# Kernel optimization log

Measured on AMD Instinct MI355X. Metric: run time of the kernel, lower is better.

## Reference

```python
import jax, jax.numpy as jnp
import numpy as np

N_NODES = 100000
N_EDGES = 800000
IN_DIM = 128
NUM_HEADS = 8
HEAD_DIM = 16  # out_dim // num_heads = 128 // 8


def setup_inputs() -> dict:
    key = jax.random.key(0)
    ks = jax.random.split(key, 10)
    scale = 1.0 / np.sqrt(IN_DIM)
    return {
        "x": jax.random.normal(ks[0], (N_NODES, IN_DIM), dtype=jnp.float32),
        "edge_index": jax.random.randint(ks[1], (2, N_EDGES), 0, N_NODES, dtype=jnp.int64),
        "virt_h": jax.random.normal(ks[2], (1, IN_DIM), dtype=jnp.float32),
        "virt_edge_index": jax.random.randint(ks[3], (2, 1), 0, 1, dtype=jnp.int64),
        "Wq": jax.random.normal(ks[4], (IN_DIM, NUM_HEADS * HEAD_DIM), dtype=jnp.float32) * scale,
        "bq": jnp.zeros((NUM_HEADS * HEAD_DIM,), dtype=jnp.float32),
        "Wk": jax.random.normal(ks[5], (IN_DIM, NUM_HEADS * HEAD_DIM), dtype=jnp.float32) * scale,
        "bk": jnp.zeros((NUM_HEADS * HEAD_DIM,), dtype=jnp.float32),
        "Wv": jax.random.normal(ks[6], (IN_DIM, NUM_HEADS * HEAD_DIM), dtype=jnp.float32) * scale,
        "bv": jnp.zeros((NUM_HEADS * HEAD_DIM,), dtype=jnp.float32),
    }


def reference(x, edge_index, virt_h, virt_edge_index, Wq, bq, Wk, bk, Wv, bv):
    # use_virt_nodes=False: virt_h / virt_edge_index are unused dummies.
    n = x.shape[0]
    H, D = NUM_HEADS, HEAD_DIM
    Q = (x @ Wq + bq).reshape(n, H, D)
    K = (x @ Wk + bk).reshape(n, H, D)
    V = (x @ Wv + bv).reshape(n, H, D)

    src = edge_index[0]
    dst = edge_index[1]

    # edge-wise gather QK dot -> clamp -> exp; score: [E, H, 1]
    dot = jnp.sum(K[src] * Q[dst], axis=-1, keepdims=True) / np.sqrt(D).astype(np.float32)
    score = jnp.exp(jnp.clip(dot, -5.0, 5.0))

    msg = V[src] * score  # [E, H, D]
    wV = jax.ops.segment_sum(msg, dst, num_segments=n)     # [N, H, D]
    Z = jax.ops.segment_sum(score, dst, num_segments=n)    # [N, H, 1]

    h_out = (wV / (Z + 1e-6)).reshape(n, H * D)
    return h_out
```

## Files before the change

### kernel.cpp

```cpp
#include <hip/hip_runtime.h>

#define IN_DIM   128
#define NH       8
#define HD       16
#define OUTD     128
#define QKVD     384

typedef unsigned short ushort_t;
typedef unsigned int   uint_t;
typedef __bf16 bf16x8 __attribute__((ext_vector_type(8)));
typedef float  f32x4  __attribute__((ext_vector_type(4)));
typedef unsigned short us4 __attribute__((ext_vector_type(4)));

__device__ __forceinline__ float bf2f(ushort_t u) {
    return __uint_as_float(((uint_t)u) << 16);
}
__device__ __forceinline__ ushort_t f2bf(float f) {
    uint_t u = __float_as_uint(f);
    u += 0x7FFFu + ((u >> 16) & 1u);
    return (ushort_t)(u >> 16);
}

__global__ __launch_bounds__(256) void prep_w(
    const float* __restrict__ Wq, const float* __restrict__ Wk,
    const float* __restrict__ Wv, ushort_t* __restrict__ Wt,
    int* __restrict__ P, unsigned long long* __restrict__ desc, int N)
{
    __shared__ float ld[32][33];
    int mat  = blockIdx.x >> 4;
    int tile = blockIdx.x & 15;
    int k0 = (tile >> 2) * 32, c0 = (tile & 3) * 32;
    const float* W = (mat == 0) ? Wq : (mat == 1) ? Wk : Wv;
    int t = threadIdx.x;
    {
        int k = t >> 3, c4 = (t & 7) * 4;
        float4 f = *(const float4*)&W[(size_t)(k0 + k) * 128 + c0 + c4];
        ld[k][c4 + 0] = f.x; ld[k][c4 + 1] = f.y;
        ld[k][c4 + 2] = f.z; ld[k][c4 + 3] = f.w;
    }
    __syncthreads();
    {
        int c = t >> 3, kg = (t & 7) * 4;
        union { ushort_t h[4]; uint2 u; } o;
        o.h[0] = f2bf(ld[kg + 0][c]); o.h[1] = f2bf(ld[kg + 1][c]);
        o.h[2] = f2bf(ld[kg + 2][c]); o.h[3] = f2bf(ld[kg + 3][c]);
        *(uint2*)&Wt[((size_t)(mat * 128 + c0 + c)) * 128 + k0 + kg] = o.u;
    }
    int t0 = blockIdx.x * 256 + threadIdx.x;
    for (int i = t0; i < N; i += 48 * 256) P[i] = 0;
    if (t0 < 128) desc[t0] = 0ULL;
}

__global__ __launch_bounds__(384, 3) void gemm_rank(
    const float* __restrict__ x, const ushort_t* __restrict__ Wt,
    const float* __restrict__ bq, const float* __restrict__ bk,
    const float* __restrict__ bv,
    const int* __restrict__ ei, int* __restrict__ P,
    ushort_t* __restrict__ rank,
    ushort_t* __restrict__ qkv,
    int N, int E, int ntiles)
{
    {
        int gtid   = (int)blockIdx.x * 384 + threadIdx.x;
        int stride = (int)gridDim.x * 384;
        for (int e = gtid; e < E; e += stride) {
            int d = ei[E + e];
            int old = atomicAdd(&P[d], 1);
            rank[e] = (ushort_t)old;
        }
    }

    __shared__ ushort_t sh[8320];

    const int tid  = threadIdx.x;
    const int w    = tid >> 6;
    const int quad = (tid >> 4) & 3;
    const int l15  = tid & 15;
    const int colg = w << 6;

    bf16x8 bfr[4][4];
#pragma unroll
    for (int kt = 0; kt < 4; kt++)
#pragma unroll
        for (int cs = 0; cs < 4; cs++) {
            int col = colg + cs * 16 + l15;
            bfr[kt][cs] = *(const bf16x8*)&Wt[(size_t)col * 128 + kt * 32 + quad * 8];
        }

    const int mat = w >> 1;
    const float* Bp = (mat == 0) ? bq : (mat == 1) ? bk : bv;
    float bias[4];
#pragma unroll
    for (int cs = 0; cs < 4; cs++)
        bias[cs] = Bp[((w & 1) << 6) + cs * 16 + l15];

    for (int tile = blockIdx.x; tile < ntiles; tile += gridDim.x) {
        const int row0 = tile * 64;
        __syncthreads();

        for (int ch = tid; ch < 1024; ch += 384) {
            int row = ch >> 4;
            int kc  = ch & 15;
            int grow = row0 + row; if (grow > N - 1) grow = N - 1;
            const float* xp = x + (size_t)grow * IN_DIM + kc * 8;
            float4 f0 = *(const float4*)xp;
            float4 f1 = *(const float4*)(xp + 4);
            union { ushort_t h[8]; uint4 u; } tt;
            tt.h[0] = f2bf(f0.x); tt.h[1] = f2bf(f0.y);
            tt.h[2] = f2bf(f0.z); tt.h[3] = f2bf(f0.w);
            tt.h[4] = f2bf(f1.x); tt.h[5] = f2bf(f1.y);
            tt.h[6] = f2bf(f1.z); tt.h[7] = f2bf(f1.w);
            *(uint4*)&sh[(kc * 65 + row) * 8] = tt.u;
        }
        __syncthreads();

        f32x4 acc[4][4];
#pragma unroll
        for (int r = 0; r < 4; r++)
#pragma unroll
            for (int cs = 0; cs < 4; cs++) acc[r][cs] = (f32x4){0.f, 0.f, 0.f, 0.f};

#pragma unroll
        for (int kt = 0; kt < 4; kt++) {
            int kc = kt * 4 + quad;
            bf16x8 af[4];
#pragma unroll
            for (int r = 0; r < 4; r++)
                af[r] = *(const bf16x8*)&sh[(kc * 65 + r * 16 + l15) * 8];
#pragma unroll
            for (int r = 0; r < 4; r++)
#pragma unroll
                for (int cs = 0; cs < 4; cs++)
                    acc[r][cs] = __builtin_amdgcn_mfma_f32_16x16x32_bf16(
                        af[r], bfr[kt][cs], acc[r][cs], 0, 0, 0);
        }

#define EPS 392
#pragma unroll
        for (int qq = 0; qq < 4; qq++) {
            __syncthreads();
            int lrow = quad << 2;
#pragma unroll
            for (int cs = 0; cs < 4; cs++) {
                int col = (w << 6) + cs * 16 + l15;
#pragma unroll
                for (int reg = 0; reg < 4; reg++)
                    sh[(lrow + reg) * EPS + col] = f2bf(acc[qq][cs][reg] + bias[cs]);
            }
            __syncthreads();
#pragma unroll
            for (int i = 0; i < 2; i++) {
                int c = tid + i * 384;
                int row = c / 48;
                int col = (c % 48) * 8;
                int grow = row0 + qq * 16 + row;
                if (grow < N) {
                    uint4 val = *(const uint4*)&sh[row * EPS + col];
                    *(uint4*)&qkv[(size_t)grow * QKVD + col] = val;
                }
            }
        }
#undef EPS
    }
}

__global__ __launch_bounds__(1024) void scan_onepass(
    int* __restrict__ P, unsigned long long* __restrict__ desc, int N)
{
    __shared__ int sdata[1024];
    __shared__ int s_prefix;
    int b = blockIdx.x;
    int i = b * 1024 + threadIdx.x;
    int v = (i < N) ? P[i] : 0;
    sdata[threadIdx.x] = v;
    __syncthreads();
    for (int off = 1; off < 1024; off <<= 1) {
        int t = (threadIdx.x >= off) ? sdata[threadIdx.x - off] : 0;
        __syncthreads();
        sdata[threadIdx.x] += t;
        __syncthreads();
    }
    int incl  = sdata[threadIdx.x];
    int total = sdata[1023];

    if (threadIdx.x == 0) {
        unsigned long long st1 = ((unsigned long long)((b == 0) ? 2 : 1) << 32)
                                 | (uint_t)total;
        __hip_atomic_store(&desc[b], st1, __ATOMIC_RELEASE, __HIP_MEMORY_SCOPE_AGENT);
        int prefix = 0;
        if (b > 0) {
            int bb = b - 1;
            for (;;) {
                unsigned long long d = __hip_atomic_load(
                    &desc[bb], __ATOMIC_ACQUIRE, __HIP_MEMORY_SCOPE_AGENT);
                uint_t st = (uint_t)(d >> 32);
                if (st == 0) continue;
                prefix += (int)(uint_t)(d & 0xFFFFFFFFu);
                if (st == 2) break;
                bb--;
            }
            __hip_atomic_store(&desc[b],
                ((unsigned long long)2 << 32) | (uint_t)(prefix + total),
                __ATOMIC_RELEASE, __HIP_MEMORY_SCOPE_AGENT);
        }
        s_prefix = prefix;
    }
    __syncthreads();
    if (i < N) P[i] = s_prefix + incl - v;
}

__global__ __launch_bounds__(256) void scatter(
    const int* __restrict__ ei, const int* __restrict__ P,
    const ushort_t* __restrict__ rank,
    int* __restrict__ sorted_src, int E)
{
    int e0 = (blockIdx.x * 256 + threadIdx.x) * 4;
    if (e0 + 4 <= E) {
        int4 s4 = *(const int4*)&ei[e0];
        int4 d4 = *(const int4*)&ei[E + e0];
        us4  r4 = *(const us4*)&rank[e0];
        sorted_src[P[d4.x] + (int)r4[0]] = s4.x;
        sorted_src[P[d4.y] + (int)r4[1]] = s4.y;
        sorted_src[P[d4.z] + (int)r4[2]] = s4.z;
        sorted_src[P[d4.w] + (int)r4[3]] = s4.w;
    } else {
        for (int e = e0; e < E; e++) {
            int pos = P[ei[E + e]] + (int)rank[e];
            sorted_src[pos] = ei[e];
        }
    }
}

__global__ __launch_bounds__(256) void segment_attn(
    const ushort_t* __restrict__ qkv,
    const int* __restrict__ P, const int* __restrict__ sorted_src,
    float* __restrict__ out, int N, int E)
{
    int n = (blockIdx.x * 256 + threadIdx.x) >> 4;
    int g = threadIdx.x & 15;
    if (n >= N) return;
    int start = P[n];
    int end   = (n + 1 < N) ? P[n + 1] : E;
    int deg   = end - start;

    const uint_t* qrow = (const uint_t*)(qkv + (size_t)n * QKVD);
    uint4 qu = *(const uint4*)(qrow + g * 4);
    float q0 = bf2f((ushort_t)(qu.x & 0xFFFF)), q1 = bf2f((ushort_t)(qu.x >> 16));
    float q2 = bf2f((ushort_t)(qu.y & 0xFFFF)), q3 = bf2f((ushort_t)(qu.y >> 16));
    float q4 = bf2f((ushort_t)(qu.z & 0xFFFF)), q5 = bf2f((ushort_t)(qu.z >> 16));
    float q6 = bf2f((ushort_t)(qu.w & 0xFFFF)), q7 = bf2f((ushort_t)(qu.w >> 16));

    float a0 = 0.f, a1 = 0.f, a2 = 0.f, a3 = 0.f;
    float a4 = 0.f, a5 = 0.f, a6 = 0.f, a7 = 0.f, z = 0.f;

    int myidx = (g < deg) ? sorted_src[start + g] : 0;
    int wbase = (threadIdx.x & 63) & 48;

#define PROC(ku, vu)                                                       \
    {                                                                      \
        float p = bf2f((ushort_t)((ku).x & 0xFFFF)) * q0                   \
                + bf2f((ushort_t)((ku).x >> 16))    * q1                   \
                + bf2f((ushort_t)((ku).y & 0xFFFF)) * q2                   \
                + bf2f((ushort_t)((ku).y >> 16))    * q3                   \
                + bf2f((ushort_t)((ku).z & 0xFFFF)) * q4                   \
                + bf2f((ushort_t)((ku).z >> 16))    * q5                   \
                + bf2f((ushort_t)((ku).w & 0xFFFF)) * q6                   \
                + bf2f((ushort_t)((ku).w >> 16))    * q7;                  \
        p += __shfl_xor(p, 1);                                             \
        p = fminf(fmaxf(p * 0.25f, -5.f), 5.f);                            \
        float s = __expf(p);                                               \
        a0 += bf2f((ushort_t)((vu).x & 0xFFFF)) * s;                       \
        a1 += bf2f((ushort_t)((vu).x >> 16))    * s;                       \
        a2 += bf2f((ushort_t)((vu).y & 0xFFFF)) * s;                       \
        a3 += bf2f((ushort_t)((vu).y >> 16))    * s;                       \
        a4 += bf2f((ushort_t)((vu).z & 0xFFFF)) * s;                       \
        a5 += bf2f((ushort_t)((vu).z >> 16))    * s;                       \
        a6 += bf2f((ushort_t)((vu).w & 0xFFFF)) * s;                       \
        a7 += bf2f((ushort_t)((vu).w >> 16))    * s;                       \
        z += s;                                                            \
    }

    int cnt = (deg < 16) ? deg : 16;
    int t = 0;
    for (; t + 2 <= cnt; t += 2) {
        int s0 = __shfl(myidx, wbase + t);
        int s1 = __shfl(myidx, wbase + t + 1);
        const uint_t* kv0 = (const uint_t*)(qkv + (size_t)s0 * QKVD + 128);
        const uint_t* kv1 = (const uint_t*)(qkv + (size_t)s1 * QKVD + 128);
        uint4 ku0 = *(const uint4*)(kv0 + g * 4);
        uint4 ku1 = *(const uint4*)(kv1 + g * 4);
        uint4 vu0 = *(const uint4*)(kv0 + 64 + g * 4);
        uint4 vu1 = *(const uint4*)(kv1 + 64 + g * 4);
        PROC(ku0, vu0); PROC(ku1, vu1);
    }
    if (t < cnt) {
        int s0 = __shfl(myidx, wbase + t);
        const uint_t* kv0 = (const uint_t*)(qkv + (size_t)s0 * QKVD + 128);
        uint4 ku0 = *(const uint4*)(kv0 + g * 4);
        uint4 vu0 = *(const uint4*)(kv0 + 64 + g * 4);
        PROC(ku0, vu0);
    }
    for (int j = start + 16; j < end; j++) {
        int s0 = sorted_src[j];
        const uint_t* kv0 = (const uint_t*)(qkv + (size_t)s0 * QKVD + 128);
        uint4 ku0 = *(const uint4*)(kv0 + g * 4);
        uint4 vu0 = *(const uint4*)(kv0 + 64 + g * 4);
        PROC(ku0, vu0);
    }
#undef PROC

    float inv = 1.f / (z + 1e-6f);
    float4 o0 = {a0 * inv, a1 * inv, a2 * inv, a3 * inv};
    float4 o1 = {a4 * inv, a5 * inv, a6 * inv, a7 * inv};
    float* ob = out + (size_t)n * OUTD + g * 8;
    *(float4*)ob = o0;
    *(float4*)(ob + 4) = o1;
}

extern "C" void kernel_launch(void* const* d_in, const int* in_sizes, int n_in,
                              void* d_out, int out_size, void* d_ws, size_t ws_size,
                              hipStream_t stream) {
    const float* x  = (const float*)d_in[0];
    const int*   ei = (const int*)d_in[1];
    const float* Wq = (const float*)d_in[4];
    const float* bq = (const float*)d_in[5];
    const float* Wk = (const float*)d_in[6];
    const float* bk = (const float*)d_in[7];
    const float* Wv = (const float*)d_in[8];
    const float* bv = (const float*)d_in[9];
    float* out = (float*)d_out;

    const int N = in_sizes[0] / IN_DIM;
    const int E = in_sizes[1] / 2;

    char* wsb = (char*)d_ws;
    ushort_t* qkv = (ushort_t*)wsb;
    ushort_t* Wt  = qkv + (size_t)N * QKVD;
    int* P = (int*)(Wt + 384 * 128);
    unsigned long long* desc = (unsigned long long*)((char*)P + (size_t)N * 4);
    int* sorted = (int*)((char*)desc + 1024);
    ushort_t* rank = (ushort_t*)(sorted + E);

    const int ntiles = (N + 63) / 64;
    const int NB     = (N + 1023) / 1024;

    prep_w<<<48, 256, 0, stream>>>(Wq, Wk, Wv, Wt, P, desc, N);
    gemm_rank<<<512, 384, 0, stream>>>(
        x, Wt, bq, bk, bv, ei, P, rank, qkv, N, E, ntiles);
    scan_onepass<<<NB, 1024, 0, stream>>>(P, desc, N);
    scatter<<<(E / 4 + 255) / 256, 256, 0, stream>>>(ei, P, rank, sorted, E);
    segment_attn<<<((size_t)N * 16 + 255) / 256, 256, 0, stream>>>(
        qkv, P, sorted, out, N, E);
}
```

Before: 284.5 us.

## Replace global-atomic counting sort with two-level bucketed sort by destination

Edge sorting by destination no longer uses per-edge global atomics plus rank arrays. It now runs a block-local histogram over 128-node buckets, a scan over the bucket-by-block table, a bucketing pass with LDS atomics that packs src and the low dst bits, and a per-bucket fine sort that writes the CSR offsets and the sorted sources. This aims to cut contended global atomics and random global scatter. In exchange it adds kernels, separates the GEMM from the edge counting so the two no longer overlap, and needs an extra bucket buffer. The packed format also assumes source indices fit in 20 bits.

```diff
diff --git a/kernel.cpp b/kernel.cpp
--- a/kernel.cpp
+++ b/kernel.cpp
@@ -5,12 +5,12 @@
 #define HD       16
 #define OUTD     128
 #define QKVD     384
+#define SH       7
 
 typedef unsigned short ushort_t;
 typedef unsigned int   uint_t;
 typedef __bf16 bf16x8 __attribute__((ext_vector_type(8)));
 typedef float  f32x4  __attribute__((ext_vector_type(4)));
-typedef unsigned short us4 __attribute__((ext_vector_type(4)));
 
 __device__ __forceinline__ float bf2f(ushort_t u) {
     return __uint_as_float(((uint_t)u) << 16);
@@ -24,7 +24,7 @@
 __global__ __launch_bounds__(256) void prep_w(
     const float* __restrict__ Wq, const float* __restrict__ Wk,
     const float* __restrict__ Wv, ushort_t* __restrict__ Wt,
-    int* __restrict__ P, unsigned long long* __restrict__ desc, int N)
+    unsigned long long* __restrict__ desc)
 {
     __shared__ float ld[32][33];
     int mat  = blockIdx.x >> 4;
@@ -47,121 +47,23 @@
         *(uint2*)&Wt[((size_t)(mat * 128 + c0 + c)) * 128 + k0 + kg] = o.u;
     }
     int t0 = blockIdx.x * 256 + threadIdx.x;
-    for (int i = t0; i < N; i += 48 * 256) P[i] = 0;
     if (t0 < 128) desc[t0] = 0ULL;
 }
 
-__global__ __launch_bounds__(384, 3) void gemm_rank(
-    const float* __restrict__ x, const ushort_t* __restrict__ Wt,
-    const float* __restrict__ bq, const float* __restrict__ bk,
-    const float* __restrict__ bv,
-    const int* __restrict__ ei, int* __restrict__ P,
-    ushort_t* __restrict__ rank,
-    ushort_t* __restrict__ qkv,
-    int N, int E, int ntiles)
-{
-    {
-        int gtid   = (int)blockIdx.x * 384 + threadIdx.x;
-        int stride = (int)gridDim.x * 384;
-        for (int e = gtid; e < E; e += stride) {
-            int d = ei[E + e];
-            int old = atomicAdd(&P[d], 1);
-            rank[e] = (ushort_t)old;
-        }
-    }
-
-    __shared__ ushort_t sh[8320];
-
-    const int tid  = threadIdx.x;
-    const int w    = tid >> 6;
-    const int quad = (tid >> 4) & 3;
-    const int l15  = tid & 15;
-    const int colg = w << 6;
-
-    bf16x8 bfr[4][4];
-#pragma unroll
-    for (int kt = 0; kt < 4; kt++)
-#pragma unroll
-        for (int cs = 0; cs < 4; cs++) {
-            int col = colg + cs * 16 + l15;
-            bfr[kt][cs] = *(const bf16x8*)&Wt[(size_t)col * 128 + kt * 32 + quad * 8];
-        }
-
-    const int mat = w >> 1;
-    const float* Bp = (mat == 0) ? bq : (mat == 1) ? bk : bv;
-    float bias[4];
-#pragma unroll
-    for (int cs = 0; cs < 4; cs++)
-        bias[cs] = Bp[((w & 1) << 6) + cs * 16 + l15];
-
-    for (int tile = blockIdx.x; tile < ntiles; tile += gridDim.x) {
-        const int row0 = tile * 64;
-        __syncthreads();
-
-        for (int ch = tid; ch < 1024; ch += 384) {
-            int row = ch >> 4;
-            int kc  = ch & 15;
-            int grow = row0 + row; if (grow > N - 1) grow = N - 1;
-            const float* xp = x + (size_t)grow * IN_DIM + kc * 8;
-            float4 f0 = *(const float4*)xp;
-            float4 f1 = *(const float4*)(xp + 4);
-            union { ushort_t h[8]; uint4 u; } tt;
-            tt.h[0] = f2bf(f0.x); tt.h[1] = f2bf(f0.y);
-            tt.h[2] = f2bf(f0.z); tt.h[3] = f2bf(f0.w);
-            tt.h[4] = f2bf(f1.x); tt.h[5] = f2bf(f1.y);
-            tt.h[6] = f2bf(f1.z); tt.h[7] = f2bf(f1.w);
-            *(uint4*)&sh[(kc * 65 + row) * 8] = tt.u;
-        }
-        __syncthreads();
-
-        f32x4 acc[4][4];
-#pragma unroll
-        for (int r = 0; r < 4; r++)
-#pragma unroll
-            for (int cs = 0; cs < 4; cs++) acc[r][cs] = (f32x4){0.f, 0.f, 0.f, 0.f};
-
-#pragma unroll
-        for (int kt = 0; kt < 4; kt++) {
-            int kc = kt * 4 + quad;
-            bf16x8 af[4];
-#pragma unroll
-            for (int r = 0; r < 4; r++)
-                af[r] = *(const bf16x8*)&sh[(kc * 65 + r * 16 + l15) * 8];
-#pragma unroll
-            for (int r = 0; r < 4; r++)
-#pragma unroll
-                for (int cs = 0; cs < 4; cs++)
-                    acc[r][cs] = __builtin_amdgcn_mfma_f32_16x16x32_bf16(
-                        af[r], bfr[kt][cs], acc[r][cs], 0, 0, 0);
-        }
-
-#define EPS 392
-#pragma unroll
-        for (int qq = 0; qq < 4; qq++) {
-            __syncthreads();
-            int lrow = quad << 2;
-#pragma unroll
-            for (int cs = 0; cs < 4; cs++) {
-                int col = (w << 6) + cs * 16 + l15;
-#pragma unroll
-                for (int reg = 0; reg < 4; reg++)
-                    sh[(lrow + reg) * EPS + col] = f2bf(acc[qq][cs][reg] + bias[cs]);
-            }
-            __syncthreads();
-#pragma unroll
-            for (int i = 0; i < 2; i++) {
-                int c = tid + i * 384;
-                int row = c / 48;
-                int col = (c % 48) * 8;
-                int grow = row0 + qq * 16 + row;
-                if (grow < N) {
-                    uint4 val = *(const uint4*)&sh[row * EPS + col];
-                    *(uint4*)&qkv[(size_t)grow * QKVD + col] = val;
-                }
-            }
-        }
-#undef EPS
-    }
+__global__ __launch_bounds__(256) void ehist(
+    const int* __restrict__ ei, int* __restrict__ Hf, int E, int NBC)
+{
+    __shared__ int lh[1024];
+    for (int i = threadIdx.x; i < 1024; i += 256) lh[i] = 0;
+    __syncthreads();
+    int CH = (E + 127) >> 7;
+    int e0 = blockIdx.x * CH;
+    int e1 = min(E, e0 + CH);
+    for (int e = e0 + threadIdx.x; e < e1; e += 256)
+        atomicAdd(&lh[ei[E + e] >> SH], 1);
+    __syncthreads();
+    for (int b = threadIdx.x; b < NBC; b += 256)
+        Hf[b * 128 + blockIdx.x] = lh[b];
 }
 
 __global__ __launch_bounds__(1024) void scan_onepass(
@@ -209,25 +111,161 @@
     if (i < N) P[i] = s_prefix + incl - v;
 }
 
-__global__ __launch_bounds__(256) void scatter(
-    const int* __restrict__ ei, const int* __restrict__ P,
-    const ushort_t* __restrict__ rank,
-    int* __restrict__ sorted_src, int E)
-{
-    int e0 = (blockIdx.x * 256 + threadIdx.x) * 4;
-    if (e0 + 4 <= E) {
-        int4 s4 = *(const int4*)&ei[e0];
-        int4 d4 = *(const int4*)&ei[E + e0];
-        us4  r4 = *(const us4*)&rank[e0];
-        sorted_src[P[d4.x] + (int)r4[0]] = s4.x;
-        sorted_src[P[d4.y] + (int)r4[1]] = s4.y;
-        sorted_src[P[d4.z] + (int)r4[2]] = s4.z;
-        sorted_src[P[d4.w] + (int)r4[3]] = s4.w;
-    } else {
-        for (int e = e0; e < E; e++) {
-            int pos = P[ei[E + e]] + (int)rank[e];
-            sorted_src[pos] = ei[e];
-        }
+__global__ __launch_bounds__(256) void ebucket(
+    const int* __restrict__ ei, const int* __restrict__ S,
+    uint_t* __restrict__ bkt, int E, int NBC)
+{
+    __shared__ int lb[1024];
+    for (int b = threadIdx.x; b < NBC; b += 256)
+        lb[b] = S[b * 128 + blockIdx.x];
+    __syncthreads();
+    int CH = (E + 127) >> 7;
+    int e0 = blockIdx.x * CH;
+    int e1 = min(E, e0 + CH);
+    for (int e = e0 + threadIdx.x; e < e1; e += 256) {
+        int d   = ei[E + e];
+        int src = ei[e];
+        int pos = atomicAdd(&lb[d >> SH], 1);
+        bkt[pos] = (uint_t)src | ((uint_t)(d & 127) << 20);
+    }
+}
+
+__global__ __launch_bounds__(256) void efine(
+    const uint_t* __restrict__ bkt, const int* __restrict__ S,
+    int* __restrict__ P, int* __restrict__ sorted_src,
+    int E, int N, int NBC)
+{
+    __shared__ int cnt[128];
+    __shared__ int scn[128];
+    int b    = blockIdx.x;
+    int base = S[b * 128];
+    int end  = (b + 1 < NBC) ? S[(b + 1) * 128] : E;
+    int m    = end - base;
+    if (threadIdx.x < 128) cnt[threadIdx.x] = 0;
+    __syncthreads();
+    for (int i = threadIdx.x; i < m; i += 256)
+        atomicAdd(&cnt[bkt[base + i] >> 20], 1);
+    __syncthreads();
+    if (threadIdx.x < 128) scn[threadIdx.x] = cnt[threadIdx.x];
+    __syncthreads();
+    for (int off = 1; off < 128; off <<= 1) {
+        int v = (threadIdx.x >= off && threadIdx.x < 128) ? scn[threadIdx.x - off] : 0;
+        __syncthreads();
+        if (threadIdx.x < 128) scn[threadIdx.x] += v;
+        __syncthreads();
+    }
+    if (threadIdx.x < 128) {
+        int excl = scn[threadIdx.x] - cnt[threadIdx.x];
+        int n = b * 128 + threadIdx.x;
+        if (n < N) P[n] = base + excl;
+        cnt[threadIdx.x] = excl;
+    }
+    __syncthreads();
+    for (int i = threadIdx.x; i < m; i += 256) {
+        uint_t r = bkt[base + i];
+        int pos = atomicAdd(&cnt[r >> 20], 1);
+        sorted_src[base + pos] = (int)(r & 0xFFFFFu);
+    }
+}
+
+__global__ __launch_bounds__(384, 3) void gemm(
+    const float* __restrict__ x, const ushort_t* __restrict__ Wt,
+    const float* __restrict__ bq, const float* __restrict__ bk,
+    const float* __restrict__ bv,
+    ushort_t* __restrict__ qkv,
+    int N, int ntiles)
+{
+    __shared__ ushort_t sh[8320];
+
+    const int tid  = threadIdx.x;
+    const int w    = tid >> 6;
+    const int quad = (tid >> 4) & 3;
+    const int l15  = tid & 15;
+    const int colg = w << 6;
+
+    bf16x8 bfr[4][4];
+#pragma unroll
+    for (int kt = 0; kt < 4; kt++)
+#pragma unroll
+        for (int cs = 0; cs < 4; cs++) {
+            int col = colg + cs * 16 + l15;
+            bfr[kt][cs] = *(const bf16x8*)&Wt[(size_t)col * 128 + kt * 32 + quad * 8];
+        }
+
+    const int mat = w >> 1;
+    const float* Bp = (mat == 0) ? bq : (mat == 1) ? bk : bv;
+    float bias[4];
+#pragma unroll
+    for (int cs = 0; cs < 4; cs++)
+        bias[cs] = Bp[((w & 1) << 6) + cs * 16 + l15];
+
+    for (int tile = blockIdx.x; tile < ntiles; tile += gridDim.x) {
+        const int row0 = tile * 64;
+        __syncthreads();
+
+        for (int ch = tid; ch < 1024; ch += 384) {
+            int row = ch >> 4;
+            int kc  = ch & 15;
+            int grow = row0 + row; if (grow > N - 1) grow = N - 1;
+            const float* xp = x + (size_t)grow * IN_DIM + kc * 8;
+            float4 f0 = *(const float4*)xp;
+            float4 f1 = *(const float4*)(xp + 4);
+            union { ushort_t h[8]; uint4 u; } tt;
+            tt.h[0] = f2bf(f0.x); tt.h[1] = f2bf(f0.y);
+            tt.h[2] = f2bf(f0.z); tt.h[3] = f2bf(f0.w);
+            tt.h[4] = f2bf(f1.x); tt.h[5] = f2bf(f1.y);
+            tt.h[6] = f2bf(f1.z); tt.h[7] = f2bf(f1.w);
+            *(uint4*)&sh[(kc * 65 + row) * 8] = tt.u;
+        }
+        __syncthreads();
+
+        f32x4 acc[4][4];
+#pragma unroll
+        for (int r = 0; r < 4; r++)
+#pragma unroll
+            for (int cs = 0; cs < 4; cs++) acc[r][cs] = (f32x4){0.f, 0.f, 0.f, 0.f};
+
+#pragma unroll
+        for (int kt = 0; kt < 4; kt++) {
+            int kc = kt * 4 + quad;
+            bf16x8 af[4];
+#pragma unroll
+            for (int r = 0; r < 4; r++)
+                af[r] = *(const bf16x8*)&sh[(kc * 65 + r * 16 + l15) * 8];
+#pragma unroll
+            for (int r = 0; r < 4; r++)
+#pragma unroll
+                for (int cs = 0; cs < 4; cs++)
+                    acc[r][cs] = __builtin_amdgcn_mfma_f32_16x16x32_bf16(
+                        af[r], bfr[kt][cs], acc[r][cs], 0, 0, 0);
+        }
+
+#define EPS 392
+#pragma unroll
+        for (int qq = 0; qq < 4; qq++) {
+            __syncthreads();
+            int lrow = quad << 2;
+#pragma unroll
+            for (int cs = 0; cs < 4; cs++) {
+                int col = (w << 6) + cs * 16 + l15;
+#pragma unroll
+                for (int reg = 0; reg < 4; reg++)
+                    sh[(lrow + reg) * EPS + col] = f2bf(acc[qq][cs][reg] + bias[cs]);
+            }
+            __syncthreads();
+#pragma unroll
+            for (int i = 0; i < 2; i++) {
+                int c = tid + i * 384;
+                int row = c / 48;
+                int col = (c % 48) * 8;
+                int grow = row0 + qq * 16 + row;
+                if (grow < N) {
+                    uint4 val = *(const uint4*)&sh[row * EPS + col];
+                    *(uint4*)&qkv[(size_t)grow * QKVD + col] = val;
+                }
+            }
+        }
+#undef EPS
     }
 }
 
@@ -332,23 +370,27 @@
 
     const int N = in_sizes[0] / IN_DIM;
     const int E = in_sizes[1] / 2;
+    const int NBC = (N + 127) >> 7;
+    const int NS  = NBC * 128;
 
     char* wsb = (char*)d_ws;
     ushort_t* qkv = (ushort_t*)wsb;
     ushort_t* Wt  = qkv + (size_t)N * QKVD;
-    int* P = (int*)(Wt + 384 * 128);
-    unsigned long long* desc = (unsigned long long*)((char*)P + (size_t)N * 4);
+    int* Hf = (int*)(Wt + 384 * 128);
+    unsigned long long* desc = (unsigned long long*)(Hf + NS);
     int* sorted = (int*)((char*)desc + 1024);
-    ushort_t* rank = (ushort_t*)(sorted + E);
+    uint_t* bkt = (uint_t*)(sorted + E);
+    int* P = (int*)(bkt + E);
 
     const int ntiles = (N + 63) / 64;
-    const int NB     = (N + 1023) / 1024;
-
-    prep_w<<<48, 256, 0, stream>>>(Wq, Wk, Wv, Wt, P, desc, N);
-    gemm_rank<<<512, 384, 0, stream>>>(
-        x, Wt, bq, bk, bv, ei, P, rank, qkv, N, E, ntiles);
-    scan_onepass<<<NB, 1024, 0, stream>>>(P, desc, N);
-    scatter<<<(E / 4 + 255) / 256, 256, 0, stream>>>(ei, P, rank, sorted, E);
+    const int NB     = (NS + 1023) / 1024;
+
+    prep_w<<<48, 256, 0, stream>>>(Wq, Wk, Wv, Wt, desc);
+    ehist<<<128, 256, 0, stream>>>(ei, Hf, E, NBC);
+    scan_onepass<<<NB, 1024, 0, stream>>>(Hf, desc, NS);
+    ebucket<<<128, 256, 0, stream>>>(ei, Hf, bkt, E, NBC);
+    efine<<<NBC, 256, 0, stream>>>(bkt, Hf, P, sorted, E, N, NBC);
+    gemm<<<512, 384, 0, stream>>>(x, Wt, bq, bk, bv, qkv, N, ntiles);
     segment_attn<<<((size_t)N * 16 + 255) / 256, 256, 0, stream>>>(
         qkv, P, sorted, out, N, E);
 }
```

Result: faster. 272.4 us (-4.2%).
